# Kernel tuning notes

Measured on AMD Instinct MI355X. Metric: run time of the kernel, lower is better.

Reference implementation:

```python
import jax, jax.numpy as jnp
import numpy as np


def setup_inputs() -> dict:
    key = jax.random.key(0)
    k1, k2, k3, k4 = jax.random.split(key, 4)
    N, M, D = 4096, 4096, 8
    x = jax.random.normal(k1, (N, D), dtype=jnp.float32)
    xx = jax.random.normal(k2, (M, D), dtype=jnp.float32)
    # raw (free-form) hyperparameters; positive() = softplus
    scale_raw = jax.random.normal(k3, (D,), dtype=jnp.float32)
    variance_raw = jax.random.normal(k4, (), dtype=jnp.float32)
    return {"x": x, "xx": xx, "scale_raw": scale_raw, "variance_raw": variance_raw}


def reference(x, xx, scale_raw, variance_raw):
    scale = jax.nn.softplus(scale_raw)          # (D,)
    variance = jax.nn.softplus(variance_raw)    # scalar
    xs = x / scale                               # (N, D)
    xxs = xx / scale                             # (M, D)
    # squared euclidean distance without materializing (N, M, D):
    # ||a-b||^2 = ||a||^2 + ||b||^2 - 2 a.b
    sq_x = jnp.sum(xs * xs, axis=-1)             # (N,)
    sq_xx = jnp.sum(xxs * xxs, axis=-1)          # (M,)
    cross = jnp.einsum("nd,md->nm", xs, xxs)    # (N, M)
    d2 = jnp.maximum(sq_x[:, None] + sq_xx[None, :] - 2.0 * cross, 0.0)
    cov = jnp.exp(-0.5 * d2) * variance          # (N, M)
    return cov
```

## Files before the change

kernel.cpp:

```cpp
#include <hip/hip_runtime.h>
#include <math.h>


#define TILE_N 16
#define BLOCK 256
#define D 8
#define M_PER_BLOCK (BLOCK * 4)

__device__ __forceinline__ float softplus_f(float z) {
    return fmaxf(z, 0.0f) + log1pf(__expf(-fabsf(z)));
}

__global__ __launch_bounds__(BLOCK) void rbf_kernel(
    const float* __restrict__ x,
    const float* __restrict__ xx,
    const float* __restrict__ scale_raw,
    const float* __restrict__ var_raw,
    float* __restrict__ out,
    int N, int M)
{
    __shared__ float s_xs[TILE_N][D];
    __shared__ float s_rscale[D];
    __shared__ float s_var;

    const int tid = threadIdx.x;
    const int m0 = blockIdx.x * M_PER_BLOCK + tid * 4;
    const int n0 = blockIdx.y * TILE_N;

    if (tid < D) {
        s_rscale[tid] = 1.0f / softplus_f(scale_raw[tid]);
    }
    if (tid == D) {
        s_var = softplus_f(var_raw[0]);
    }
    __syncthreads();

    if (tid < TILE_N * D) {
        const int r = tid / D, c = tid % D;
        s_xs[r][c] = x[(n0 + r) * D + c] * s_rscale[c];
    }
    __syncthreads();

    float rs[D];
#pragma unroll
    for (int d = 0; d < D; ++d) rs[d] = s_rscale[d];

    float b[4][D];
    const float* xxp = xx + (size_t)m0 * D;
#pragma unroll
    for (int j = 0; j < 4; ++j) {
        const float4 lo = *(const float4*)(xxp + j * D);
        const float4 hi = *(const float4*)(xxp + j * D + 4);
        b[j][0] = lo.x * rs[0]; b[j][1] = lo.y * rs[1];
        b[j][2] = lo.z * rs[2]; b[j][3] = lo.w * rs[3];
        b[j][4] = hi.x * rs[4]; b[j][5] = hi.y * rs[5];
        b[j][6] = hi.z * rs[6]; b[j][7] = hi.w * rs[7];
    }

    const float var = s_var;

#pragma unroll
    for (int n = 0; n < TILE_N; ++n) {
        float a[D];
#pragma unroll
        for (int d = 0; d < D; ++d) a[d] = s_xs[n][d];

        float4 r;
        float* rp = &r.x;
#pragma unroll
        for (int j = 0; j < 4; ++j) {
            float d2 = 0.0f;
#pragma unroll
            for (int d = 0; d < D; ++d) {
                const float t = a[d] - b[j][d];
                d2 = fmaf(t, t, d2);
            }
            rp[j] = var * __expf(-0.5f * d2);
        }
        *(float4*)(out + (size_t)(n0 + n) * M + m0) = r;
    }
}

extern "C" void kernel_launch(void* const* d_in, const int* in_sizes, int n_in,
                              void* d_out, int out_size, void* d_ws, size_t ws_size,
                              hipStream_t stream) {
    const float* x    = (const float*)d_in[0];
    const float* xx   = (const float*)d_in[1];
    const float* sraw = (const float*)d_in[2];
    const float* vraw = (const float*)d_in[3];
    float* out = (float*)d_out;

    const int N = in_sizes[0] / D;
    const int M = in_sizes[1] / D;

    dim3 grid(M / M_PER_BLOCK, N / TILE_N);
    rbf_kernel<<<grid, BLOCK, 0, stream>>>(x, xx, sraw, vraw, out, N, M);
}
```

Measured before the change: 87.21 us.

## Expand squared distance into dot-product form with packed FMA and exp2

Rewrites the distance as c_n - h_m + a·b with log2(e) and log2(variance) folded into the precomputed terms. The inner loop then becomes one packed fp32 FMA per dimension per two columns, followed by a single exp2 with no extra multiply. Output stores switch to nontemporal vector stores so the write stream bypasses cache retention. This trades the numerically exact difference-of-squares form for the expanded form, which can cancel in fp32, and relies on the fminf clamp in place of the max(d2,0) guard.

```diff
diff --git a/kernel.cpp b/kernel.cpp
--- a/kernel.cpp
+++ b/kernel.cpp
@@ -7,8 +7,15 @@
 #define D 8
 #define M_PER_BLOCK (BLOCK * 4)
 
+typedef float v2f __attribute__((ext_vector_type(2)));
+typedef float v4f __attribute__((ext_vector_type(4)));
+
 __device__ __forceinline__ float softplus_f(float z) {
     return fmaxf(z, 0.0f) + log1pf(__expf(-fabsf(z)));
+}
+
+__device__ __forceinline__ float fast_exp2(float z) {
+    return __builtin_exp2f(z);
 }
 
 __global__ __launch_bounds__(BLOCK) void rbf_kernel(
@@ -19,65 +26,93 @@
     float* __restrict__ out,
     int N, int M)
 {
-    __shared__ float s_xs[TILE_N][D];
-    __shared__ float s_rscale[D];
-    __shared__ float s_var;
+    __shared__ float s_a[TILE_N][D];
+    __shared__ float s_c[TILE_N];
+    __shared__ float s_rs[D];
+    __shared__ float s_l2v;
 
     const int tid = threadIdx.x;
     const int m0 = blockIdx.x * M_PER_BLOCK + tid * 4;
     const int n0 = blockIdx.y * TILE_N;
 
     if (tid < D) {
-        s_rscale[tid] = 1.0f / softplus_f(scale_raw[tid]);
+        s_rs[tid] = 1.2011224087864498f / softplus_f(scale_raw[tid]);
     }
     if (tid == D) {
-        s_var = softplus_f(var_raw[0]);
+        s_l2v = log2f(softplus_f(var_raw[0]));
     }
     __syncthreads();
 
     if (tid < TILE_N * D) {
-        const int r = tid / D, c = tid % D;
-        s_xs[r][c] = x[(n0 + r) * D + c] * s_rscale[c];
+        const int r = tid >> 3, c = tid & 7;
+        s_a[r][c] = x[(n0 + r) * D + c] * s_rs[c];
+    }
+
+    float rs[D];
+#pragma unroll
+    for (int d = 0; d < D; ++d) rs[d] = s_rs[d];
+
+    v2f b01[D], b23[D];
+    {
+        const float* xxp = xx + (size_t)m0 * D;
+        float bj[4][D];
+#pragma unroll
+        for (int j = 0; j < 4; ++j) {
+            const float4 lo = *(const float4*)(xxp + j * D);
+            const float4 hi = *(const float4*)(xxp + j * D + 4);
+            bj[j][0] = lo.x * rs[0]; bj[j][1] = lo.y * rs[1];
+            bj[j][2] = lo.z * rs[2]; bj[j][3] = lo.w * rs[3];
+            bj[j][4] = hi.x * rs[4]; bj[j][5] = hi.y * rs[5];
+            bj[j][6] = hi.z * rs[6]; bj[j][7] = hi.w * rs[7];
+        }
+#pragma unroll
+        for (int d = 0; d < D; ++d) {
+            b01[d] = (v2f){bj[0][d], bj[1][d]};
+            b23[d] = (v2f){bj[2][d], bj[3][d]};
+        }
+    }
+    v2f h01 = {0.f, 0.f}, h23 = {0.f, 0.f};
+#pragma unroll
+    for (int d = 0; d < D; ++d) {
+        h01 = __builtin_elementwise_fma(b01[d], b01[d], h01);
+        h23 = __builtin_elementwise_fma(b23[d], b23[d], h23);
+    }
+    h01 *= 0.5f; h23 *= 0.5f;
+
+    __syncthreads();
+
+    if (tid < TILE_N) {
+        float s = 0.f;
+#pragma unroll
+        for (int d = 0; d < D; ++d) s = fmaf(s_a[tid][d], s_a[tid][d], s);
+        s_c[tid] = s_l2v - 0.5f * s;
     }
     __syncthreads();
 
-    float rs[D];
-#pragma unroll
-    for (int d = 0; d < D; ++d) rs[d] = s_rscale[d];
-
-    float b[4][D];
-    const float* xxp = xx + (size_t)m0 * D;
-#pragma unroll
-    for (int j = 0; j < 4; ++j) {
-        const float4 lo = *(const float4*)(xxp + j * D);
-        const float4 hi = *(const float4*)(xxp + j * D + 4);
-        b[j][0] = lo.x * rs[0]; b[j][1] = lo.y * rs[1];
-        b[j][2] = lo.z * rs[2]; b[j][3] = lo.w * rs[3];
-        b[j][4] = hi.x * rs[4]; b[j][5] = hi.y * rs[5];
-        b[j][6] = hi.z * rs[6]; b[j][7] = hi.w * rs[7];
-    }
-
-    const float var = s_var;
+    const float l2v = s_l2v;
 
 #pragma unroll
     for (int n = 0; n < TILE_N; ++n) {
-        float a[D];
+        const float4 alo = *(const float4*)&s_a[n][0];
+        const float4 ahi = *(const float4*)&s_a[n][4];
+        const float c = s_c[n];
+        const float a_[D] = {alo.x, alo.y, alo.z, alo.w, ahi.x, ahi.y, ahi.z, ahi.w};
+
+        v2f acc01 = (v2f){c, c} - h01;
+        v2f acc23 = (v2f){c, c} - h23;
 #pragma unroll
-        for (int d = 0; d < D; ++d) a[d] = s_xs[n][d];
+        for (int d = 0; d < D; ++d) {
+            const v2f av = (v2f){a_[d], a_[d]};
+            acc01 = __builtin_elementwise_fma(av, b01[d], acc01);
+            acc23 = __builtin_elementwise_fma(av, b23[d], acc23);
+        }
 
-        float4 r;
-        float* rp = &r.x;
-#pragma unroll
-        for (int j = 0; j < 4; ++j) {
-            float d2 = 0.0f;
-#pragma unroll
-            for (int d = 0; d < D; ++d) {
-                const float t = a[d] - b[j][d];
-                d2 = fmaf(t, t, d2);
-            }
-            rp[j] = var * __expf(-0.5f * d2);
-        }
-        *(float4*)(out + (size_t)(n0 + n) * M + m0) = r;
+        v4f r;
+        r.x = fast_exp2(fminf(acc01.x, l2v));
+        r.y = fast_exp2(fminf(acc01.y, l2v));
+        r.z = fast_exp2(fminf(acc23.x, l2v));
+        r.w = fast_exp2(fminf(acc23.y, l2v));
+        __builtin_nontemporal_store(r, (v4f*)(out + (size_t)(n0 + n) * M + m0));
     }
 }
 
```

Measured after the change: 86.20 us. Within noise of the previous version (-1.2%).
